# Performance work log

Measured on AMD Instinct MI355X. Metric: run time of the kernel, lower is better.

Reference implementation:

```python
import jax, jax.numpy as jnp
import numpy as np

N = 20000      # nodes
E = 320000     # edges (avg degree 16)
IN = 512       # input feature dim
HID = 64       # hidden_dim
NH = 8         # n_heads
NC = 20        # n_classes
NG = 64        # graphs in batch
EPS = 1e-5     # batchnorm eps


def setup_inputs() -> dict:
    key = jax.random.key(0)
    ks = jax.random.split(key, 32)
    rn = lambda k, shape, s=0.05: (jax.random.normal(k, shape, jnp.float32) * s)
    inp = {
        "x": rn(ks[0], (N, IN), 1.0),
        "src": jax.random.randint(ks[1], (E,), 0, N),
        "dst": jax.random.randint(ks[2], (E,), 0, N),
        "graph_ids": jnp.sort(jax.random.randint(ks[3], (N,), 0, NG)),
        "n_graphs": NG,
        # encoder
        "W_enc": rn(ks[4], (IN, HID)), "b_enc": jnp.zeros((HID,), jnp.float32),
        # GAT layer 0
        "fc_W0": rn(ks[5], (HID, NH * HID)),
        "attn_l0": rn(ks[6], (NH, HID)), "attn_r0": rn(ks[7], (NH, HID)),
        "res_W0": rn(ks[8], (HID, NH * HID)),
        "bias0": jnp.zeros((NH * HID,), jnp.float32),
        "dp_W0": rn(ks[9], (NH * HID, HID)), "dp_b0": jnp.zeros((HID,), jnp.float32),
        # GAT layer 1
        "fc_W1": rn(ks[10], (HID, NH * HID)),
        "attn_l1": rn(ks[11], (NH, HID)), "attn_r1": rn(ks[12], (NH, HID)),
        "res_W1": rn(ks[13], (HID, NH * HID)),
        "bias1": jnp.zeros((NH * HID,), jnp.float32),
        "dp_W1": rn(ks[14], (NH * HID, HID)), "dp_b1": jnp.zeros((HID,), jnp.float32),
        # batchnorm affine
        "gamma": jnp.ones((2 * HID,), jnp.float32), "beta": jnp.zeros((2 * HID,), jnp.float32),
        # global attention pooling gate
        "gate_W": rn(ks[15], (2 * HID, 1)), "gate_b": jnp.zeros((1,), jnp.float32),
        # classifier
        "cls_W": rn(ks[16], (2 * HID, NC)), "cls_b": jnp.zeros((NC,), jnp.float32),
    }
    return inp


def gat_conv(h, fc_W, attn_l, attn_r, res_W, bias, src, dst, n_nodes):
    # DGL GATConv: fc -> per-head scalar scores -> edge softmax over incoming
    # edges -> weighted sum -> residual + bias -> leaky_relu activation.
    nh, d = attn_l.shape
    feat = (h @ fc_W).reshape(n_nodes, nh, d)              # [N,H,D]
    el = jnp.sum(feat * attn_l[None], axis=-1)             # [N,H]
    er = jnp.sum(feat * attn_r[None], axis=-1)             # [N,H]
    e = jax.nn.leaky_relu(el[src] + er[dst], 0.2)          # [E,H]
    m = jax.ops.segment_max(e, dst, num_segments=n_nodes)  # segment softmax
    ex = jnp.exp(e - m[dst])
    denom = jax.ops.segment_sum(ex, dst, num_segments=n_nodes)
    a = ex / denom[dst]                                    # [E,H]
    msg = feat[src] * a[:, :, None]                        # [E,H,D]  (dominant)
    rst = jax.ops.segment_sum(msg, dst, num_segments=n_nodes)  # [N,H,D]
    rst = rst + (h @ res_W).reshape(n_nodes, nh, d) + bias.reshape(nh, d)
    return jax.nn.leaky_relu(rst, 0.01)  # F.leaky_relu default slope


def reference(x, W_enc, b_enc,
              fc_W0, attn_l0, attn_r0, res_W0, bias0, dp_W0, dp_b0,
              fc_W1, attn_l1, attn_r1, res_W1, bias1, dp_W1, dp_b1,
              gamma, beta, gate_W, gate_b, cls_W, cls_b,
              src, dst, graph_ids, n_graphs):
    n_nodes = x.shape[0]
    he = x @ W_enc + b_enc                                  # encoder [N,HID]
    h = he
    h = gat_conv(h, fc_W0, attn_l0, attn_r0, res_W0, bias0, src, dst, n_nodes)
    h = h.reshape(n_nodes, -1) @ dp_W0 + dp_b0              # down_proj 0
    h = gat_conv(h, fc_W1, attn_l1, attn_r1, res_W1, bias1, src, dst, n_nodes)
    h = h.reshape(n_nodes, -1) @ dp_W1 + dp_b1              # down_proj 1
    hg = jnp.concatenate([h, he], axis=1)                   # [N,2*HID]
    # BatchNorm1d (training-mode batch stats, biased variance)
    mu = jnp.mean(hg, axis=0)
    var = jnp.var(hg, axis=0)
    hg = (hg - mu) * jax.lax.rsqrt(var + EPS) * gamma + beta
    # GlobalAttentionPooling: per-graph softmax over node gates
    gate = hg @ gate_W + gate_b                             # [N,1]
    gm = jax.ops.segment_max(gate, graph_ids, num_segments=n_graphs)
    ge = jnp.exp(gate - gm[graph_ids])
    gden = jax.ops.segment_sum(ge, graph_ids, num_segments=n_graphs)
    alpha = ge / gden[graph_ids]                            # [N,1]
    readout = jax.ops.segment_sum(alpha * hg, graph_ids, num_segments=n_graphs)
    return readout @ cls_W + cls_b                          # [NG,NC]
```

## Files before the change

kernel.cpp:

```cpp
#include <hip/hip_runtime.h>
#include <hip/hip_bf16.h>

#define MROWS   20000
#define N_EDGES 320000
#define DIN     512
#define HID     64
#define NH      8
#define ND      512
#define NCLS    20
#define NG      64
#define BN_EPS  1e-5f
#define PCH     16
#define BNB     256

typedef __hip_bfloat16 bf16;
typedef __attribute__((ext_vector_type(8))) short s16x8;
typedef __attribute__((ext_vector_type(4))) float f32x4;

enum { TF32 = 0, TBF16 = 1, TMODE = 2 };

__device__ __forceinline__ float ld_f32(const void* p, size_t i) { return ((const float*)p)[i]; }
__device__ __forceinline__ float ld_b16(const void* p, size_t i) { return __bfloat162float(((const bf16*)p)[i]); }

template<int T>
__device__ __forceinline__ float ldT(const void* p, size_t i, int bf) {
    if constexpr (T == TF32) return ld_f32(p, i);
    else if constexpr (T == TBF16) return ld_b16(p, i);
    else return bf ? ld_b16(p, i) : ld_f32(p, i);
}
template<int T>
__device__ __forceinline__ void stT(void* p, size_t i, int bf, float v) {
    if constexpr (T == TF32) ((float*)p)[i] = v;
    else if constexpr (T == TBF16) ((bf16*)p)[i] = __float2bfloat16(v);
    else { if (bf) ((bf16*)p)[i] = __float2bfloat16(v); else ((float*)p)[i] = v; }
}

__global__ void detect_kernel(const void* __restrict__ gamma, int* __restrict__ mode) {
    if (threadIdx.x == 0 && blockIdx.x == 0)
        *mode = (*(const unsigned*)gamma == 0x3F800000u) ? 0 : 1;
}

struct TP { const void* src[7]; bf16* dst[7]; int K[7]; };
__global__ void transpose7_kernel(TP tp, const int* __restrict__ modep) {
    const int bf = *modep;
    int id = blockIdx.y;
    int i = blockIdx.x * 256 + threadIdx.x;
    int K = tp.K[id];
    int N = (DIN * HID) / K;
    int n = i / K, k = i - n * K;
    tp.dst[id][i] = __float2bfloat16(ldT<TMODE>(tp.src[id], (size_t)k * N + n, bf));
}

__global__ void convx_kernel(const void* __restrict__ x, bf16* __restrict__ xb,
                             const int* __restrict__ modep) {
    if (*modep) return;
    int i = (blockIdx.x * 256 + threadIdx.x) * 4;
    if (i >= MROWS * DIN) return;
    float4 v = ((const float4*)x)[i >> 2];
    xb[i + 0] = __float2bfloat16(v.x);
    xb[i + 1] = __float2bfloat16(v.y);
    xb[i + 2] = __float2bfloat16(v.z);
    xb[i + 3] = __float2bfloat16(v.w);
}

__global__ void hist_kernel(const int* __restrict__ keys, int* __restrict__ counts, int n) {
    int i = blockIdx.x * 256 + threadIdx.x;
    if (i < n) atomicAdd(&counts[keys[i]], 1);
}

__global__ void gsearch_kernel(const int* __restrict__ gids, int* __restrict__ goffs) {
    int g = threadIdx.x;
    if (g > NG) return;
    int lo = 0, hi = MROWS;
    while (lo < hi) {
        int mid = (lo + hi) >> 1;
        if (gids[mid] < g) lo = mid + 1; else hi = mid;
    }
    goffs[g] = lo;
}

__global__ __launch_bounds__(1024)
void scan1_kernel(const int* __restrict__ in, int* __restrict__ out,
                  int* __restrict__ partial, int n) {
    int i = blockIdx.x * 1024 + threadIdx.x;
    int v = (i < n) ? in[i] : 0;
    int lane = threadIdx.x & 63, wid = threadIdx.x >> 6;
    int s = v;
    #pragma unroll
    for (int o = 1; o < 64; o <<= 1) { int t = __shfl_up(s, o, 64); if (lane >= o) s += t; }
    __shared__ int wsum[16];
    if (lane == 63) wsum[wid] = s;
    __syncthreads();
    if (wid == 0 && lane < 16) {
        int t = wsum[lane];
        #pragma unroll
        for (int o = 1; o < 16; o <<= 1) { int u = __shfl_up(t, o, 64); if (lane >= o) t += u; }
        wsum[lane] = t;
    }
    __syncthreads();
    int carry = (wid > 0) ? wsum[wid - 1] : 0;
    int incl = s + carry;
    if (i < n) out[i] = incl - v;
    if (threadIdx.x == 1023) partial[blockIdx.x] = incl;
}

__global__ void scan2_kernel(int* __restrict__ partial, int nb) {
    int l = threadIdx.x;
    int v = (l < nb) ? partial[l] : 0;
    int s = v;
    #pragma unroll
    for (int o = 1; o < 64; o <<= 1) { int t = __shfl_up(s, o, 64); if (l >= o) s += t; }
    if (l < nb) partial[l] = s - v;
}

__global__ __launch_bounds__(1024)
void scan3_kernel(int* __restrict__ out, const int* __restrict__ partial, int n, int total) {
    int i = blockIdx.x * 1024 + threadIdx.x;
    if (i < n) out[i] += partial[blockIdx.x];
    if (i == 0) out[n] = total;
}

__global__ void scatter_kernel(const int* __restrict__ src, const int* __restrict__ dst,
                               const int* __restrict__ offs, int* __restrict__ cursor,
                               int* __restrict__ src_sorted) {
    int e = blockIdx.x * 256 + threadIdx.x;
    if (e < N_EDGES) {
        int d = dst[e];
        int pos = offs[d] + atomicAdd(&cursor[d], 1);
        src_sorted[pos] = src[e];
    }
}

template<int K, int NB, int NTOT>
__global__ __launch_bounds__(256)
void gemm_mfma(const void* __restrict__ Araw, const bf16* __restrict__ Aconv,
               const bf16* __restrict__ BT, const void* __restrict__ bias,
               bf16* __restrict__ C, const int* __restrict__ modep) {
    const int bf = *modep;
    const bf16* A = bf ? (const bf16*)Araw : Aconv;
    const int wid  = threadIdx.x >> 6;
    const int lane = threadIdx.x & 63;
    const int quad = lane >> 4;
    const int l16  = lane & 15;
    const int rb = blockIdx.x * 128 + wid * 32;
    const int cb = blockIdx.y * NB;
    constexpr int CT = NB / 16;
    constexpr int KC = K / 32;

    f32x4 acc[2][CT] = {};
    int r0 = rb + l16;       if (r0 >= MROWS) r0 = MROWS - 1;
    int r1 = rb + 16 + l16;  if (r1 >= MROWS) r1 = MROWS - 1;
    const bf16* a0p = A + (size_t)r0 * K + quad * 8;
    const bf16* a1p = A + (size_t)r1 * K + quad * 8;
    const bf16* btp = BT + (size_t)(cb + l16) * K + quad * 8;

    for (int kc = 0; kc < KC; ++kc) {
        s16x8 af0 = *(const s16x8*)(a0p + kc * 32);
        s16x8 af1 = *(const s16x8*)(a1p + kc * 32);
        s16x8 bfr[CT];
        #pragma unroll
        for (int ct = 0; ct < CT; ++ct)
            bfr[ct] = *(const s16x8*)(btp + (size_t)ct * 16 * K + kc * 32);
        #pragma unroll
        for (int ct = 0; ct < CT; ++ct) {
            acc[0][ct] = __builtin_amdgcn_mfma_f32_16x16x32_bf16(af0, bfr[ct], acc[0][ct], 0, 0, 0);
            acc[1][ct] = __builtin_amdgcn_mfma_f32_16x16x32_bf16(af1, bfr[ct], acc[1][ct], 0, 0, 0);
        }
    }
    #pragma unroll
    for (int ct = 0; ct < CT; ++ct) {
        int col = cb + ct * 16 + l16;
        float bb = bias ? ldT<TMODE>(bias, col, bf) : 0.f;
        #pragma unroll
        for (int rt = 0; rt < 2; ++rt) {
            #pragma unroll
            for (int rg = 0; rg < 4; ++rg) {
                int row = rb + rt * 16 + quad * 4 + rg;
                if (row < MROWS)
                    C[(size_t)row * NTOT + col] = __float2bfloat16(acc[rt][ct][rg] + bb);
            }
        }
    }
}

__global__ void elr_kernel(const bf16* __restrict__ feat, const void* __restrict__ attn_l,
                           const void* __restrict__ attn_r, float* __restrict__ el,
                           float* __restrict__ er, const int* __restrict__ modep) {
    const int bf = *modep;
    int i = blockIdx.x * 256 + threadIdx.x;
    if (i >= MROWS * NH) return;
    int n = i >> 3, h = i & 7;
    const s16x8* f8 = (const s16x8*)(feat + (size_t)n * ND + h * HID);
    float al = 0.f, ar = 0.f;
    for (int c = 0; c < 8; ++c) {
        s16x8 fv = f8[c];
        #pragma unroll
        for (int j = 0; j < 8; ++j) {
            float fvf = __uint_as_float(((unsigned)(unsigned short)fv[j]) << 16);
            int d = c * 8 + j;
            al += fvf * ldT<TMODE>(attn_l, h * HID + d, bf);
            ar += fvf * ldT<TMODE>(attn_r, h * HID + d, bf);
        }
    }
    el[i] = al;
    er[i] = ar;
}

__global__ __launch_bounds__(256)
void agg_kernel(const bf16* __restrict__ feat, const float* __restrict__ el,
                const float* __restrict__ er, const int* __restrict__ offs,
                const int* __restrict__ srcs, bf16* __restrict__ rst) {
    int gid = blockIdx.x * 256 + threadIdx.x;
    int n = gid >> 6;
    int lane = threadIdx.x & 63;
    if (n >= MROWS) return;
    int e0 = offs[n], e1 = offs[n + 1];
    int hl = lane & 7;
    float er_l = er[n * 8 + hl];
    float acc[8] = {0.f, 0.f, 0.f, 0.f, 0.f, 0.f, 0.f, 0.f};
    float den[8] = {0.f, 0.f, 0.f, 0.f, 0.f, 0.f, 0.f, 0.f};
    for (int e = e0; e < e1; ++e) {
        int s = srcs[e];
        float sc = el[s * 8 + hl] + er_l;
        sc = sc > 0.f ? sc : 0.2f * sc;
        float wv = __expf(fminf(sc, 30.f));
        const bf16* fs = feat + (size_t)s * ND;
        #pragma unroll
        for (int h = 0; h < 8; ++h) {
            float wgt = __shfl(wv, h, 64);
            den[h] += wgt;
            acc[h] += __bfloat162float(fs[h * 64 + lane]) * wgt;
        }
    }
    size_t base = (size_t)n * ND + lane;
    #pragma unroll
    for (int h = 0; h < 8; ++h) {
        float v = (den[h] > 0.f) ? acc[h] / den[h] : 0.f;
        float r = __bfloat162float(rst[base + h * 64]) + v;
        rst[base + h * 64] = __float2bfloat16(r > 0.f ? r : 0.01f * r);
    }
}

__global__ void bn_part_kernel(const bf16* __restrict__ h2, const bf16* __restrict__ he,
                               float* __restrict__ psum, float* __restrict__ psq) {
    int t = threadIdx.x;
    int b = blockIdx.x;
    int beg = (int)((long)MROWS * b / BNB);
    int end = (int)((long)MROWS * (b + 1) / BNB);
    const bf16* srcb = (t < 64) ? h2 : he;
    int col = t & 63;
    float s = 0.f, s2 = 0.f;
    for (int r = beg; r < end; ++r) {
        float v = __bfloat162float(srcb[(size_t)r * 64 + col]);
        s += v;
        s2 += v * v;
    }
    psum[b * 128 + t] = s;
    psq[b * 128 + t] = s2;
}

__global__ void bn_reduce_kernel(const float* __restrict__ psum, const float* __restrict__ psq,
                                 const void* __restrict__ gamma, const void* __restrict__ beta,
                                 float* __restrict__ scale, float* __restrict__ shift,
                                 const int* __restrict__ modep) {
    const int bf = *modep;
    int t = threadIdx.x;
    float s = 0.f, s2 = 0.f;
    for (int b = 0; b < BNB; ++b) { s += psum[b * 128 + t]; s2 += psq[b * 128 + t]; }
    float mu = s * (1.f / MROWS);
    float var = s2 * (1.f / MROWS) - mu * mu;
    float inv = rsqrtf(fmaxf(var, 0.f) + BN_EPS);
    float a = ldT<TMODE>(gamma, t, bf) * inv;
    scale[t] = a;
    shift[t] = ldT<TMODE>(beta, t, bf) - mu * a;
}

__global__ __launch_bounds__(256)
void gate_kernel(const bf16* __restrict__ h2, const bf16* __restrict__ he,
                 const float* __restrict__ scale, const float* __restrict__ shift,
                 const void* __restrict__ gate_W, const void* __restrict__ gate_b,
                 float* __restrict__ ge, const int* __restrict__ modep) {
    const int bf = *modep;
    int gid = blockIdx.x * 256 + threadIdx.x;
    int r = gid >> 6;
    int l = threadIdx.x & 63;
    if (r >= MROWS) return;
    float v0 = __bfloat162float(h2[(size_t)r * 64 + l]) * scale[l] + shift[l];
    float v1 = __bfloat162float(he[(size_t)r * 64 + l]) * scale[64 + l] + shift[64 + l];
    float s = v0 * ldT<TMODE>(gate_W, l, bf) + v1 * ldT<TMODE>(gate_W, 64 + l, bf);
    #pragma unroll
    for (int o = 32; o > 0; o >>= 1) s += __shfl_xor(s, o, 64);
    if (l == 0) {
        float g = s + ldT<TMODE>(gate_b, 0, bf);
        ge[r] = __expf(fminf(fmaxf(g, -60.f), 30.f));
    }
}

__global__ void pool1_kernel(const bf16* __restrict__ h2, const bf16* __restrict__ he,
                             const float* __restrict__ scale, const float* __restrict__ shift,
                             const float* __restrict__ ge, const int* __restrict__ goffs,
                             float* __restrict__ pacc, float* __restrict__ pden) {
    int g = blockIdx.x;
    int c = blockIdx.y;
    int t = threadIdx.x;
    int r0 = goffs[g], r1 = goffs[g + 1];
    int len = r1 - r0;
    int beg = r0 + (int)((long)len * c / PCH);
    int end = r0 + (int)((long)len * (c + 1) / PCH);
    const bf16* srcb = (t < 64) ? h2 : he;
    int col = t & 63;
    float sc = scale[t], sh = shift[t];
    float acc = 0.f, den = 0.f;
    for (int r = beg; r < end; ++r) {
        float wg = ge[r];
        float v = __bfloat162float(srcb[(size_t)r * 64 + col]) * sc + sh;
        den += wg;
        acc += wg * v;
    }
    pacc[((size_t)g * PCH + c) * 128 + t] = acc;
    if (t == 0) pden[g * PCH + c] = den;
}

__global__ void pool2_kernel(const float* __restrict__ pacc, const float* __restrict__ pden,
                             float* __restrict__ readout) {
    int g = blockIdx.x;
    int t = threadIdx.x;
    float acc = 0.f, den = 0.f;
    #pragma unroll
    for (int c = 0; c < PCH; ++c) {
        acc += pacc[((size_t)g * PCH + c) * 128 + t];
        den += pden[g * PCH + c];
    }
    readout[g * 128 + t] = (den > 0.f) ? acc / den : 0.f;
}

__global__ void cls_kernel(const float* __restrict__ readout, const void* __restrict__ W,
                           const void* __restrict__ b, void* __restrict__ out,
                           const int* __restrict__ modep) {
    const int bf = *modep;
    int i = blockIdx.x * 256 + threadIdx.x;
    if (i >= NG * NCLS) return;
    int g = i / NCLS, c = i - g * NCLS;
    float acc = ldT<TMODE>(b, c, bf);
    #pragma unroll 8
    for (int k = 0; k < 128; ++k)
        acc += readout[g * 128 + k] * ldT<TMODE>(W, k * NCLS + c, bf);
    stT<TMODE>(out, i, bf, acc);
}

extern "C" void kernel_launch(void* const* d_in, const int* in_sizes, int n_in,
                              void* d_out, int out_size, void* d_ws, size_t ws_size,
                              hipStream_t stream) {
    const void* x       = d_in[0];
    const int*  src     = (const int*)d_in[1];
    const int*  dst     = (const int*)d_in[2];
    const int*  gids    = (const int*)d_in[3];
    const void* W_enc   = d_in[5];
    const void* b_enc   = d_in[6];
    const void* fc_W0   = d_in[7];
    const void* attn_l0 = d_in[8];
    const void* attn_r0 = d_in[9];
    const void* res_W0  = d_in[10];
    const void* bias0   = d_in[11];
    const void* dp_W0   = d_in[12];
    const void* dp_b0   = d_in[13];
    const void* fc_W1   = d_in[14];
    const void* attn_l1 = d_in[15];
    const void* attn_r1 = d_in[16];
    const void* res_W1  = d_in[17];
    const void* bias1   = d_in[18];
    const void* dp_W1   = d_in[19];
    const void* dp_b1   = d_in[20];
    const void* gamma   = d_in[21];
    const void* beta    = d_in[22];
    const void* gate_W  = d_in[23];
    const void* gate_b  = d_in[24];
    const void* cls_W   = d_in[25];
    const void* cls_b   = d_in[26];

    char* wsc = (char*)d_ws;
    size_t off = 0;
    auto alloc = [&](size_t bytes) -> void* {
        void* p = wsc + off;
        off = (off + bytes + 255) & ~(size_t)255;
        return p;
    };
    bf16*  he        = (bf16*) alloc((size_t)MROWS * HID * 2);
    bf16*  h         = (bf16*) alloc((size_t)MROWS * HID * 2);
    bf16*  h2        = (bf16*) alloc((size_t)MROWS * HID * 2);
    bf16*  feat      = (bf16*) alloc((size_t)MROWS * ND * 2);
    bf16*  rst       = (bf16*) alloc((size_t)MROWS * ND * 2);
    bf16*  xb        = rst;
    bf16*  bt_enc    = (bf16*) alloc((size_t)DIN * HID * 2);
    bf16*  bt_fc0    = (bf16*) alloc((size_t)HID * ND * 2);
    bf16*  bt_res0   = (bf16*) alloc((size_t)HID * ND * 2);
    bf16*  bt_dp0    = (bf16*) alloc((size_t)ND * HID * 2);
    bf16*  bt_fc1    = (bf16*) alloc((size_t)HID * ND * 2);
    bf16*  bt_res1   = (bf16*) alloc((size_t)HID * ND * 2);
    bf16*  bt_dp1    = (bf16*) alloc((size_t)ND * HID * 2);
    float* el        = (float*)alloc((size_t)MROWS * 8 * 4);
    float* er        = (float*)alloc((size_t)MROWS * 8 * 4);
    float* ge        = (float*)alloc((size_t)MROWS * 4);
    float* readout   = (float*)alloc((size_t)NG * 128 * 4);
    int*   src_sorted= (int*)  alloc((size_t)N_EDGES * 4);
    int*   offs      = (int*)  alloc((size_t)(MROWS + 1) * 4);
    int*   goffs     = (int*)  alloc((size_t)(NG + 1) * 4);
    int*   spartial  = (int*)  alloc(64 * 4);
    float* psum      = (float*)alloc((size_t)BNB * 128 * 4);
    float* psq       = (float*)alloc((size_t)BNB * 128 * 4);
    float* pacc      = (float*)alloc((size_t)NG * PCH * 128 * 4);
    float* pden      = (float*)alloc((size_t)NG * PCH * 4);
    float* bnscale   = (float*)alloc(128 * 4);
    float* bnshift   = (float*)alloc(128 * 4);
    int*   mode      = (int*)  alloc(4);
    size_t zbytes = (size_t)MROWS * 4 * 2;
    char*  zbase  = (char*)alloc(zbytes);
    int* counts  = (int*)zbase;
    int* cursor  = counts + MROWS;

    hipMemsetAsync(zbase, 0, zbytes, stream);
    detect_kernel<<<1, 64, 0, stream>>>(gamma, mode);

    TP tp;
    tp.src[0] = W_enc;  tp.K[0] = DIN;
    tp.src[1] = fc_W0;  tp.K[1] = HID;
    tp.src[2] = res_W0; tp.K[2] = HID;
    tp.src[3] = dp_W0;  tp.K[3] = ND;
    tp.src[4] = fc_W1;  tp.K[4] = HID;
    tp.src[5] = res_W1; tp.K[5] = HID;
    tp.src[6] = dp_W1;  tp.K[6] = ND;
    tp.dst[0] = bt_enc; tp.dst[1] = bt_fc0; tp.dst[2] = bt_res0; tp.dst[3] = bt_dp0;
    tp.dst[4] = bt_fc1; tp.dst[5] = bt_res1; tp.dst[6] = bt_dp1;
    transpose7_kernel<<<dim3((DIN * HID) / 256, 7), 256, 0, stream>>>(tp, mode);
    convx_kernel<<<(MROWS * DIN / 4 + 255) / 256, 256, 0, stream>>>(x, xb, mode);

    hist_kernel<<<(N_EDGES + 255) / 256, 256, 0, stream>>>(dst, counts, N_EDGES);
    gsearch_kernel<<<1, 128, 0, stream>>>(gids, goffs);
    const int SB = (MROWS + 1023) / 1024;
    scan1_kernel<<<SB, 1024, 0, stream>>>(counts, offs, spartial, MROWS);
    scan2_kernel<<<1, 64, 0, stream>>>(spartial, SB);
    scan3_kernel<<<SB, 1024, 0, stream>>>(offs, spartial, MROWS, N_EDGES);
    scatter_kernel<<<(N_EDGES + 255) / 256, 256, 0, stream>>>(src, dst, offs, cursor, src_sorted);

    const int GX = (MROWS + 127) / 128;

    gemm_mfma<DIN, 64, 64><<<dim3(GX, 1), 256, 0, stream>>>(x, xb, bt_enc, b_enc, he, mode);

    gemm_mfma<HID, 128, ND><<<dim3(GX, 4), 256, 0, stream>>>(he, he, bt_fc0, nullptr, feat, mode);
    elr_kernel<<<(MROWS * NH) / 256, 256, 0, stream>>>(feat, attn_l0, attn_r0, el, er, mode);
    gemm_mfma<HID, 128, ND><<<dim3(GX, 4), 256, 0, stream>>>(he, he, bt_res0, bias0, rst, mode);
    agg_kernel<<<(MROWS * 64) / 256, 256, 0, stream>>>(feat, el, er, offs, src_sorted, rst);
    gemm_mfma<ND, 64, 64><<<dim3(GX, 1), 256, 0, stream>>>(rst, rst, bt_dp0, dp_b0, h, mode);

    gemm_mfma<HID, 128, ND><<<dim3(GX, 4), 256, 0, stream>>>(h, h, bt_fc1, nullptr, feat, mode);
    elr_kernel<<<(MROWS * NH) / 256, 256, 0, stream>>>(feat, attn_l1, attn_r1, el, er, mode);
    gemm_mfma<HID, 128, ND><<<dim3(GX, 4), 256, 0, stream>>>(h, h, bt_res1, bias1, rst, mode);
    agg_kernel<<<(MROWS * 64) / 256, 256, 0, stream>>>(feat, el, er, offs, src_sorted, rst);
    gemm_mfma<ND, 64, 64><<<dim3(GX, 1), 256, 0, stream>>>(rst, rst, bt_dp1, dp_b1, h2, mode);

    bn_part_kernel<<<BNB, 128, 0, stream>>>(h2, he, psum, psq);
    bn_reduce_kernel<<<1, 128, 0, stream>>>(psum, psq, gamma, beta, bnscale, bnshift, mode);
    gate_kernel<<<(MROWS * 64 + 255) / 256, 256, 0, stream>>>(h2, he, bnscale, bnshift, gate_W, gate_b, ge, mode);
    pool1_kernel<<<dim3(NG, PCH), 128, 0, stream>>>(h2, he, bnscale, bnshift, ge, goffs, pacc, pden);
    pool2_kernel<<<NG, 128, 0, stream>>>(pacc, pden, readout);
    cls_kernel<<<(NG * NCLS + 255) / 256, 256, 0, stream>>>(readout, cls_W, cls_b, d_out, mode);
}
```

Measured before the change: 556.6 us.

## Fuse fc/res GEMMs with attention score epilogue and vectorize aggregation

The fc and residual projections now run in one launch with an 8-wide grid, and the el/er attention dot products are computed in the GEMM epilogue from the accumulators. This removes the separate elr kernel and its re-read of the feature matrix. The aggregation kernel is restructured so each lane handles 8 contiguous dims of one head. Source indices are loaded 64 at a time and broadcast via shuffle, and features are read as 16-byte vectors, cutting per-edge scalar loads and shuffles. The risk is the el/er score computed from fp32 accumulators rather than bf16-rounded features, plus higher register pressure in the fused kernel.

```diff
diff --git a/kernel.cpp b/kernel.cpp
--- a/kernel.cpp
+++ b/kernel.cpp
@@ -33,6 +33,14 @@
     if constexpr (T == TF32) ((float*)p)[i] = v;
     else if constexpr (T == TBF16) ((bf16*)p)[i] = __float2bfloat16(v);
     else { if (bf) ((bf16*)p)[i] = __float2bfloat16(v); else ((float*)p)[i] = v; }
+}
+
+__device__ __forceinline__ float bfbits2f(short s) {
+    return __uint_as_float(((unsigned)(unsigned short)s) << 16);
+}
+__device__ __forceinline__ short f2bfbits(float v) {
+    bf16 b = __float2bfloat16(v);
+    return *reinterpret_cast<short*>(&b);
 }
 
 __global__ void detect_kernel(const void* __restrict__ gamma, int* __restrict__ mode) {
@@ -183,27 +191,98 @@
     }
 }
 
-__global__ void elr_kernel(const bf16* __restrict__ feat, const void* __restrict__ attn_l,
-                           const void* __restrict__ attn_r, float* __restrict__ el,
-                           float* __restrict__ er, const int* __restrict__ modep) {
+__global__ __launch_bounds__(256)
+void gemm_fcres(const bf16* __restrict__ A, const bf16* __restrict__ BT_fc,
+                const bf16* __restrict__ BT_res, const void* __restrict__ bias,
+                const void* __restrict__ attn_l, const void* __restrict__ attn_r,
+                bf16* __restrict__ feat, bf16* __restrict__ rst,
+                float* __restrict__ el, float* __restrict__ er,
+                const int* __restrict__ modep) {
     const int bf = *modep;
-    int i = blockIdx.x * 256 + threadIdx.x;
-    if (i >= MROWS * NH) return;
-    int n = i >> 3, h = i & 7;
-    const s16x8* f8 = (const s16x8*)(feat + (size_t)n * ND + h * HID);
-    float al = 0.f, ar = 0.f;
-    for (int c = 0; c < 8; ++c) {
-        s16x8 fv = f8[c];
-        #pragma unroll
-        for (int j = 0; j < 8; ++j) {
-            float fvf = __uint_as_float(((unsigned)(unsigned short)fv[j]) << 16);
-            int d = c * 8 + j;
-            al += fvf * ldT<TMODE>(attn_l, h * HID + d, bf);
-            ar += fvf * ldT<TMODE>(attn_r, h * HID + d, bf);
-        }
-    }
-    el[i] = al;
-    er[i] = ar;
+    const bool isres = blockIdx.y >= 4;
+    const int yy = blockIdx.y & 3;
+    const bf16* BT = isres ? BT_res : BT_fc;
+    bf16* C = isres ? rst : feat;
+    const int wid  = threadIdx.x >> 6;
+    const int lane = threadIdx.x & 63;
+    const int quad = lane >> 4;
+    const int l16  = lane & 15;
+    const int rb = blockIdx.x * 128 + wid * 32;
+    const int cb = yy * 128;
+    constexpr int CT = 8;
+    constexpr int K  = HID;
+    constexpr int KC = K / 32;
+
+    f32x4 acc[2][CT] = {};
+    int r0 = rb + l16;       if (r0 >= MROWS) r0 = MROWS - 1;
+    int r1 = rb + 16 + l16;  if (r1 >= MROWS) r1 = MROWS - 1;
+    const bf16* a0p = A + (size_t)r0 * K + quad * 8;
+    const bf16* a1p = A + (size_t)r1 * K + quad * 8;
+    const bf16* btp = BT + (size_t)(cb + l16) * K + quad * 8;
+
+    #pragma unroll
+    for (int kc = 0; kc < KC; ++kc) {
+        s16x8 af0 = *(const s16x8*)(a0p + kc * 32);
+        s16x8 af1 = *(const s16x8*)(a1p + kc * 32);
+        s16x8 bfr[CT];
+        #pragma unroll
+        for (int ct = 0; ct < CT; ++ct)
+            bfr[ct] = *(const s16x8*)(btp + (size_t)ct * 16 * K + kc * 32);
+        #pragma unroll
+        for (int ct = 0; ct < CT; ++ct) {
+            acc[0][ct] = __builtin_amdgcn_mfma_f32_16x16x32_bf16(af0, bfr[ct], acc[0][ct], 0, 0, 0);
+            acc[1][ct] = __builtin_amdgcn_mfma_f32_16x16x32_bf16(af1, bfr[ct], acc[1][ct], 0, 0, 0);
+        }
+    }
+    #pragma unroll
+    for (int ct = 0; ct < CT; ++ct) {
+        int col = cb + ct * 16 + l16;
+        float bb = isres ? ldT<TMODE>(bias, col, bf) : 0.f;
+        #pragma unroll
+        for (int rt = 0; rt < 2; ++rt) {
+            #pragma unroll
+            for (int rg = 0; rg < 4; ++rg) {
+                int row = rb + rt * 16 + quad * 4 + rg;
+                if (row < MROWS)
+                    C[(size_t)row * ND + col] = __float2bfloat16(acc[rt][ct][rg] + bb);
+            }
+        }
+    }
+    if (!isres) {
+        float al[CT], ar[CT];
+        #pragma unroll
+        for (int ct = 0; ct < CT; ++ct) {
+            int col = cb + ct * 16 + l16;
+            al[ct] = ldT<TMODE>(attn_l, col, bf);
+            ar[ct] = ldT<TMODE>(attn_r, col, bf);
+        }
+        #pragma unroll
+        for (int rt = 0; rt < 2; ++rt) {
+            #pragma unroll
+            for (int rg = 0; rg < 4; ++rg) {
+                float e0 = 0.f, e1 = 0.f, f0 = 0.f, f1 = 0.f;
+                #pragma unroll
+                for (int ct = 0; ct < 4; ++ct) {
+                    e0 += acc[rt][ct][rg] * al[ct];
+                    f0 += acc[rt][ct][rg] * ar[ct];
+                    e1 += acc[rt][ct + 4][rg] * al[ct + 4];
+                    f1 += acc[rt][ct + 4][rg] * ar[ct + 4];
+                }
+                #pragma unroll
+                for (int o = 1; o < 16; o <<= 1) {
+                    e0 += __shfl_xor(e0, o, 64);
+                    e1 += __shfl_xor(e1, o, 64);
+                    f0 += __shfl_xor(f0, o, 64);
+                    f1 += __shfl_xor(f1, o, 64);
+                }
+                int row = rb + rt * 16 + quad * 4 + rg;
+                if (row < MROWS) {
+                    if (l16 == 0) { el[row * 8 + 2 * yy] = e0;     er[row * 8 + 2 * yy] = f0; }
+                    if (l16 == 1) { el[row * 8 + 2 * yy + 1] = e1; er[row * 8 + 2 * yy + 1] = f1; }
+                }
+            }
+        }
+    }
 }
 
 __global__ __launch_bounds__(256)
@@ -212,33 +291,39 @@
                 const int* __restrict__ srcs, bf16* __restrict__ rst) {
     int gid = blockIdx.x * 256 + threadIdx.x;
     int n = gid >> 6;
-    int lane = threadIdx.x & 63;
+    int l = threadIdx.x & 63;
     if (n >= MROWS) return;
+    int hh = l >> 3;
     int e0 = offs[n], e1 = offs[n + 1];
-    int hl = lane & 7;
-    float er_l = er[n * 8 + hl];
+    float er_h = er[n * 8 + hh];
     float acc[8] = {0.f, 0.f, 0.f, 0.f, 0.f, 0.f, 0.f, 0.f};
-    float den[8] = {0.f, 0.f, 0.f, 0.f, 0.f, 0.f, 0.f, 0.f};
-    for (int e = e0; e < e1; ++e) {
-        int s = srcs[e];
-        float sc = el[s * 8 + hl] + er_l;
-        sc = sc > 0.f ? sc : 0.2f * sc;
-        float wv = __expf(fminf(sc, 30.f));
-        const bf16* fs = feat + (size_t)s * ND;
-        #pragma unroll
-        for (int h = 0; h < 8; ++h) {
-            float wgt = __shfl(wv, h, 64);
-            den[h] += wgt;
-            acc[h] += __bfloat162float(fs[h * 64 + lane]) * wgt;
-        }
-    }
-    size_t base = (size_t)n * ND + lane;
-    #pragma unroll
-    for (int h = 0; h < 8; ++h) {
-        float v = (den[h] > 0.f) ? acc[h] / den[h] : 0.f;
-        float r = __bfloat162float(rst[base + h * 64]) + v;
-        rst[base + h * 64] = __float2bfloat16(r > 0.f ? r : 0.01f * r);
-    }
+    float den = 0.f;
+    for (int base = e0; base < e1; base += 64) {
+        int cnt = min(64, e1 - base);
+        int sv = (base + l < e1) ? srcs[base + l] : 0;
+        for (int e = 0; e < cnt; ++e) {
+            int s = __shfl(sv, e, 64);
+            float sc = el[s * 8 + hh] + er_h;
+            sc = sc > 0.f ? sc : 0.2f * sc;
+            float w = __expf(fminf(sc, 30.f));
+            s16x8 f8 = *(const s16x8*)(feat + (size_t)s * ND + l * 8);
+            den += w;
+            #pragma unroll
+            for (int j = 0; j < 8; ++j)
+                acc[j] += bfbits2f(f8[j]) * w;
+        }
+    }
+    float inv = (den > 0.f) ? 1.f / den : 0.f;
+    s16x8* rp = (s16x8*)(rst + (size_t)n * ND + l * 8);
+    s16x8 rr = *rp;
+    s16x8 ro;
+    #pragma unroll
+    for (int j = 0; j < 8; ++j) {
+        float r = bfbits2f(rr[j]) + acc[j] * inv;
+        r = r > 0.f ? r : 0.01f * r;
+        ro[j] = f2bfbits(r);
+    }
+    *rp = ro;
 }
 
 __global__ void bn_part_kernel(const bf16* __restrict__ h2, const bf16* __restrict__ he,
@@ -446,15 +531,13 @@
 
     gemm_mfma<DIN, 64, 64><<<dim3(GX, 1), 256, 0, stream>>>(x, xb, bt_enc, b_enc, he, mode);
 
-    gemm_mfma<HID, 128, ND><<<dim3(GX, 4), 256, 0, stream>>>(he, he, bt_fc0, nullptr, feat, mode);
-    elr_kernel<<<(MROWS * NH) / 256, 256, 0, stream>>>(feat, attn_l0, attn_r0, el, er, mode);
-    gemm_mfma<HID, 128, ND><<<dim3(GX, 4), 256, 0, stream>>>(he, he, bt_res0, bias0, rst, mode);
+    gemm_fcres<<<dim3(GX, 8), 256, 0, stream>>>(he, bt_fc0, bt_res0, bias0, attn_l0, attn_r0,
+                                                feat, rst, el, er, mode);
     agg_kernel<<<(MROWS * 64) / 256, 256, 0, stream>>>(feat, el, er, offs, src_sorted, rst);
     gemm_mfma<ND, 64, 64><<<dim3(GX, 1), 256, 0, stream>>>(rst, rst, bt_dp0, dp_b0, h, mode);
 
-    gemm_mfma<HID, 128, ND><<<dim3(GX, 4), 256, 0, stream>>>(h, h, bt_fc1, nullptr, feat, mode);
-    elr_kernel<<<(MROWS * NH) / 256, 256, 0, stream>>>(feat, attn_l1, attn_r1, el, er, mode);
-    gemm_mfma<HID, 128, ND><<<dim3(GX, 4), 256, 0, stream>>>(h, h, bt_res1, bias1, rst, mode);
+    gemm_fcres<<<dim3(GX, 8), 256, 0, stream>>>(h, bt_fc1, bt_res1, bias1, attn_l1, attn_r1,
+                                                feat, rst, el, er, mode);
     agg_kernel<<<(MROWS * 64) / 256, 256, 0, stream>>>(feat, el, er, offs, src_sorted, rst);
     gemm_mfma<ND, 64, 64><<<dim3(GX, 1), 256, 0, stream>>>(rst, rst, bt_dp1, dp_b1, h2, mode);
 
```

Measured after the change: 479.2 us. 1.16x faster.
